# Performance work log

Hardware: AMD Instinct MI355X
Metric: run time of the kernel (lower is better)

The kernel has to match this reference:

```python
import jax, jax.numpy as jnp
import numpy as np
import math

B, C, H, W = 16, 128, 64, 64

def _conv3(x, w, b):
    # 3x3 conv, padding=1 (SAME), NCHW / OIHW
    y = jax.lax.conv_general_dilated(x, w, window_strides=(1, 1), padding='SAME',
                                     dimension_numbers=('NCHW', 'OIHW', 'NCHW'))
    return y + b[None, :, None, None]

def setup_inputs() -> dict:
    key = jax.random.key(0)
    ks = jax.random.split(key, 12)
    s = 0.02
    inp = {
        'F_in': jax.random.normal(ks[0], (B, C, H, W), dtype=jnp.float32),
        'Pspe': jax.random.normal(ks[1], (B, C, C), dtype=jnp.float32),
        'q_w': jax.random.normal(ks[2], (C, C, 3, 3), dtype=jnp.float32) * s,
        'q_b': jnp.zeros((C,), dtype=jnp.float32),
        'k_w': jax.random.normal(ks[3], (C, C, 3, 3), dtype=jnp.float32) * s,
        'k_b': jnp.zeros((C,), dtype=jnp.float32),
        'v_w': jax.random.normal(ks[4], (C, C, 3, 3), dtype=jnp.float32) * s,
        'v_b': jnp.zeros((C,), dtype=jnp.float32),
        'f1_w': jax.random.normal(ks[5], (C, C, 3, 3), dtype=jnp.float32) * s,
        'f1_b': jnp.zeros((C,), dtype=jnp.float32),
        'f2_w': jax.random.normal(ks[6], (C, C, 3, 3), dtype=jnp.float32) * s,
        'f2_b': jnp.zeros((C,), dtype=jnp.float32),
    }
    return inp

def reference(F_in, Pspe, q_w, q_b, k_w, k_b, v_w, v_b, f1_w, f1_b, f2_w, f2_b):
    b, c, h, w = F_in.shape
    hw = h * w
    Qm = _conv3(F_in, q_w, q_b)
    Km = _conv3(F_in, k_w, k_b)
    Vm = _conv3(F_in, v_w, v_b)
    # (B,C,H,W) -> (B,HW,C)
    Q = jnp.transpose(Qm, (0, 2, 3, 1)).reshape(b, hw, c)
    K = jnp.transpose(Km, (0, 2, 3, 1)).reshape(b, hw, c)
    V = jnp.transpose(Vm, (0, 2, 3, 1)).reshape(b, hw, c)
    # channel-wise attention: (B,C,C) = K^T Q, contracting over HW
    attn_logits = jnp.einsum('bnc,bnd->bcd', K, Q) / math.sqrt(hw)
    A = jax.nn.softmax(attn_logits, axis=-1)
    M = jnp.einsum('bce,bed->bcd', Pspe, A)         # prompt fusion
    F3 = jnp.einsum('bnc,bcd->bnd', V, M)           # (B,HW,C)
    F3_map = jnp.transpose(F3.reshape(b, h, w, c), (0, 3, 1, 2))
    # MScanBlock is not defined in the provided source -> identity
    F_ssm = F3_map
    ffn = _conv3(jax.nn.gelu(_conv3(F_ssm, f1_w, f1_b), approximate=False), f2_w, f2_b)
    return F_ssm + ffn
```

## Files before the change

### kernel.cpp

```cpp
#include <hip/hip_runtime.h>
#include <cmath>

typedef unsigned short u16;
typedef __bf16 bf16x8 __attribute__((ext_vector_type(8)));
typedef float f32x4 __attribute__((ext_vector_type(4)));

__device__ __forceinline__ u16 f2bf(float f) {
  unsigned u = __float_as_uint(f);
  u += 0x7fffu + ((u >> 16) & 1u);
  return (u16)(u >> 16);
}
__device__ __forceinline__ float bf2f(u16 h) {
  return __uint_as_float(((unsigned)h) << 16);
}
__device__ __forceinline__ f32x4 mfma_bf16(bf16x8 a, bf16x8 b, f32x4 c) {
  return __builtin_amdgcn_mfma_f32_16x16x32_bf16(a, b, c, 0, 0, 0);
}
__device__ __forceinline__ float gelu_exact(float x) {
  return 0.5f * x * (1.0f + erff(x * 0.70710678118654752440f));
}

#define VMCNT2() asm volatile("s_waitcnt vmcnt(2)" ::: "memory")
#define VMCNT0() asm volatile("s_waitcnt vmcnt(0)" ::: "memory")
#define BARR()                                  \
  do {                                          \
    asm volatile("" ::: "memory");              \
    __builtin_amdgcn_s_barrier();               \
    asm volatile("" ::: "memory");              \
  } while (0)

__device__ __forceinline__ void gload16(const void* g, void* l) {
  __builtin_amdgcn_global_load_lds(
      (const __attribute__((address_space(1))) unsigned*)g,
      (__attribute__((address_space(3))) unsigned*)l, 16, 0, 0);
}

__device__ __forceinline__ size_t pidx(int b, int y, int x) {
  return ((size_t)(b * 66 + y) * 66 + x) * 128;
}

__device__ __forceinline__ void border_yx(int k, int& y, int& x) {
  if (k < 66) { y = 0; x = k; }
  else if (k < 132) { y = 65; x = k - 66; }
  else if (k < 196) { y = k - 131; x = 0; }
  else { y = k - 195; x = 65; }
}

__global__ __launch_bounds__(256) void pack_xw(
    const float* __restrict__ Fin, u16* __restrict__ Xp,
    const float* __restrict__ w0, const float* __restrict__ w1,
    const float* __restrict__ w2, const float* __restrict__ w3,
    const float* __restrict__ w4, u16* __restrict__ Wpk) {
  const int tid = threadIdx.x;
  const int bid = blockIdx.x;
  if (bid < 1024) {
    __shared__ float T[64 * 129];
    const int b = bid >> 6, y = bid & 63;
#pragma unroll
    for (int i = 0; i < 32; ++i) {
      int idx = tid + i * 256;
      int c = idx >> 6, x = idx & 63;
      T[x * 129 + c] = Fin[(size_t)(b * 128 + c) * 4096 + y * 64 + x];
    }
    __syncthreads();
#pragma unroll
    for (int i = 0; i < 4; ++i) {
      int chunk = tid + i * 256;
      int x = chunk >> 4;
      int c0 = (chunk & 15) * 8;
      u16 tmp[8];
#pragma unroll
      for (int e = 0; e < 8; ++e) tmp[e] = f2bf(T[x * 129 + c0 + e]);
      *reinterpret_cast<uint4*>(Xp + pidx(b, y + 1, x + 1) + c0) =
          *reinterpret_cast<const uint4*>(tmp);
    }
  } else if (bid < 1384) {
    int gid = (bid - 1024) * 256 + tid;
    int lane = gid & 63;
    int nblk = (gid >> 6) & 7;
    int step = (gid >> 9) % 36;
    int conv = gid / (512 * 36);
    if (conv >= 5) return;
    const float* w = conv == 0 ? w0 : conv == 1 ? w1 : conv == 2 ? w2 : conv == 3 ? w3 : w4;
    int tap = step >> 2, cc = step & 3;
    int dy = tap / 3, dx = tap % 3;
    int co = nblk * 16 + (lane & 15);
    int ci0 = cc * 32 + (lane >> 4) * 8;
    u16 tmp[8];
#pragma unroll
    for (int e = 0; e < 8; ++e)
      tmp[e] = f2bf(w[((size_t)(co * 128 + ci0 + e) * 3 + dy) * 3 + dx]);
    size_t off = ((size_t)conv * 36 * 8 * 64 + (size_t)((step * 8 + nblk) * 64 + lane)) * 8;
    *reinterpret_cast<uint4*>(Wpk + off) = *reinterpret_cast<const uint4*>(tmp);
  } else {
    int p = (bid - 1384) * 16 + (tid >> 4);
    int b = p / 260, k = p % 260;
    int y, x;
    border_yx(k, y, x);
    *reinterpret_cast<uint4*>(Xp + pidx(b, y, x) + (tid & 15) * 8) =
        make_uint4(0u, 0u, 0u, 0u);
  }
}

template <int MODE>
__global__ __launch_bounds__(256, 2) void conv5(
    const u16* __restrict__ Xin, const u16* __restrict__ Wp0,
    const float* __restrict__ bq, const float* __restrict__ bk,
    const float* __restrict__ bv,
    u16* __restrict__ O0, u16* __restrict__ O1, u16* __restrict__ O2,
    float* __restrict__ OutF, const u16* __restrict__ Resid) {
  __shared__ alignas(16) char smem[58368];
  char* Abuf = smem;
  char* Bring = smem + 33792;
  const int tid = threadIdx.x;
  const int lane = tid & 63, wv = tid >> 6;
  const int wm = wv >> 1, wn = wv & 1;
  const int lm = lane & 15, lq = lane >> 4;
  const int bid = blockIdx.x;
  const int cv = (MODE == 0) ? (bid >> 9) : 0;
  const int mtr = bid & 511;
  const int mt = (mtr & 7) * 64 + (mtr >> 3);
  const int b = mt >> 5, yp = mt & 31;
  const u16* WpC = Wp0 + (size_t)cv * 147456;

  f32x4 acc[4][4];
#pragma unroll
  for (int i = 0; i < 4; ++i)
#pragma unroll
    for (int j = 0; j < 4; ++j) acc[i][j] = f32x4{0.f, 0.f, 0.f, 0.f};

  auto stageA = [&](int h) {
#pragma unroll
    for (int r = 0; r < 9; ++r) {
      int c = wv * 528 + r * 64 + lane;
      int row = c >> 3, c16 = c & 7;
      int ys = row / 66, xs = row - ys * 66;
      const u16* src =
          Xin + pidx(b, yp * 2 + ys, xs) + h * 64 + ((c16 ^ (xs & 7)) << 3);
      char* dst = Abuf + (wv * 528 + r * 64) * 16;
      if (r < 8)
        gload16(src, dst);
      else if (lane < 16)
        gload16(src, dst);
    }
  };
  auto stageB = [&](int t, int h) {
    int ws = (t >> 1) * 4 + h * 2 + (t & 1);
    const u16* s0 = WpC + (size_t)ws * 4096 + (size_t)(wv * 128 + lane) * 8;
    char* d0 = Bring + (t % 3) * 8192 + wv * 2048;
    gload16(s0, d0);
    gload16(s0 + 512, d0 + 1024);
  };

#pragma unroll 1
  for (int h = 0; h < 2; ++h) {
    BARR();
    stageA(h);
    stageB(0, h);
    stageB(1, h);
    VMCNT2();
    BARR();
#pragma unroll
    for (int t = 0; t < 18; ++t) {
      if (t > 0) {
        if (t < 17) VMCNT2(); else VMCNT0();
        BARR();
      }
      if (t + 2 < 18) stageB(t + 2, h);
      const int tap = t >> 1, ccL = t & 1;
      const int dy = tap / 3, dx = tap % 3;
      bf16x8 af[4], bfr[4];
#pragma unroll
      for (int i = 0; i < 4; ++i) {
        int p = wm * 64 + i * 16 + lm;
        int xs = (p & 63) + dx, ys = (p >> 6) + dy;
        unsigned off = (unsigned)(((ys * 66 + xs) * 64 + ccL * 32 + lq * 8) * 2) ^
                       (unsigned)((xs & 7) << 4);
        af[i] = *reinterpret_cast<const bf16x8*>(Abuf + off);
      }
      const char* bb = Bring + (t % 3) * 8192;
#pragma unroll
      for (int j = 0; j < 4; ++j)
        bfr[j] = *reinterpret_cast<const bf16x8*>(
            bb + ((wn * 4 + j) * 64 + lane) * 16);
#pragma unroll
      for (int i = 0; i < 4; ++i)
#pragma unroll
        for (int j = 0; j < 4; ++j) acc[i][j] = mfma_bf16(af[i], bfr[j], acc[i][j]);
    }
  }

  __syncthreads();

  if (MODE == 0 && cv < 2) {
    const float* bias = cv == 0 ? bq : bk;
    u16* OutB = cv == 0 ? O0 : O1;
    u16* T = (u16*)smem;
#pragma unroll
    for (int i = 0; i < 4; ++i)
#pragma unroll
      for (int j = 0; j < 4; ++j) {
        int n = wn * 64 + j * 16 + lm;
        float bs = bias[n];
#pragma unroll
        for (int r = 0; r < 4; ++r) {
          int m = wm * 64 + i * 16 + lq * 4 + r;
          T[n * 136 + m] = f2bf(acc[i][j][r] + bs);
        }
      }
    __syncthreads();
#pragma unroll
    for (int it = 0; it < 8; ++it) {
      int item = tid + it * 256;
      int l = item & 63, cb = (item >> 6) & 7, ksl = item >> 9;
      int c = cb * 16 + (l & 15);
      int mloc = ksl * 32 + (l >> 4) * 8;
      int ks = yp * 4 + ksl;
      *reinterpret_cast<uint4*>(
          OutB + (size_t)(((b * 128 + ks) * 8 + cb) * 64 + l) * 8) =
          *reinterpret_cast<const uint4*>(T + c * 136 + mloc);
    }
  } else if (MODE == 0) {
    u16* T = (u16*)smem;
#pragma unroll
    for (int i = 0; i < 4; ++i)
#pragma unroll
      for (int j = 0; j < 4; ++j) {
        int n = wn * 64 + j * 16 + lm;
        float bs = bv[n];
#pragma unroll
        for (int r = 0; r < 4; ++r) {
          int m = wm * 64 + i * 16 + lq * 4 + r;
          T[m * 136 + n] = f2bf(acc[i][j][r] + bs);
        }
      }
    __syncthreads();
    int rr = tid >> 1, hf = tid & 1;
    const uint4* src = reinterpret_cast<const uint4*>(T + rr * 136 + hf * 64);
    uint4* dst = reinterpret_cast<uint4*>(O2 + ((size_t)(mt * 128 + rr) * 128 + hf * 64));
#pragma unroll
    for (int k = 0; k < 8; ++k) dst[k] = src[k];
  } else if (MODE == 1) {
    u16* T = (u16*)smem;
#pragma unroll
    for (int i = 0; i < 4; ++i)
#pragma unroll
      for (int j = 0; j < 4; ++j) {
        int n = wn * 64 + j * 16 + lm;
        float bs = bq[n];
#pragma unroll
        for (int r = 0; r < 4; ++r) {
          int m = wm * 64 + i * 16 + lq * 4 + r;
          T[m * 136 + n] = f2bf(gelu_exact(acc[i][j][r] + bs));
        }
      }
    __syncthreads();
    int rr = tid >> 1, hf = tid & 1;
    int y = yp * 2 + (rr >> 6), x = rr & 63;
    const uint4* src = reinterpret_cast<const uint4*>(T + rr * 136 + hf * 64);
    uint4* dst = reinterpret_cast<uint4*>(O0 + pidx(b, y + 1, x + 1) + hf * 64);
#pragma unroll
    for (int k = 0; k < 8; ++k) dst[k] = src[k];
  } else {
    float* Tf = (float*)smem;
#pragma unroll
    for (int jh = 0; jh < 2; ++jh) {
      if (jh) __syncthreads();
#pragma unroll
      for (int i = 0; i < 4; ++i)
#pragma unroll
        for (int j2 = 0; j2 < 2; ++j2) {
          int j = jh * 2 + j2;
          int n = wn * 64 + j * 16 + lm;
          int nl = wn * 32 + j2 * 16 + lm;
          float bs = bq[n];
          int m0 = wm * 64 + i * 16 + lq * 4;
          int y = yp * 2 + (m0 >> 6), x = m0 & 63;
          const u16* rp = Resid + pidx(b, y + 1, x + 1) + n;
#pragma unroll
          for (int r = 0; r < 4; ++r)
            Tf[nl * 132 + m0 + r] = acc[i][j][r] + bs + bf2f(rp[r * 128]);
        }
      __syncthreads();
      int nl = tid >> 2, seg = tid & 3;
      int gn = (nl >> 5) * 64 + jh * 32 + (nl & 31);
      float* dst = OutF + ((size_t)(b * 128 + gn) * 4096 + yp * 128 + seg * 32);
      const float* src = Tf + nl * 132 + seg * 32;
#pragma unroll
      for (int k = 0; k < 8; ++k)
        reinterpret_cast<float4*>(dst)[k] = reinterpret_cast<const float4*>(src)[k];
    }
  }
}

__global__ __launch_bounds__(256, 2) void attn_s(const u16* __restrict__ QP,
                                                 const u16* __restrict__ KP,
                                                 float* __restrict__ SP) {
  const int tid = threadIdx.x;
  const int lane = tid & 63;
  const int wv = tid >> 6, wm = wv >> 1, wn = wv & 1;
  const int lm = lane & 15, lq = lane >> 4;
  int mt = blockIdx.x;
  mt = (mt & 7) * 16 + (mt >> 3);
  const int b = mt >> 3, sp = mt & 7;

  f32x4 acc[4][4];
#pragma unroll
  for (int i = 0; i < 4; ++i)
#pragma unroll
    for (int j = 0; j < 4; ++j) acc[i][j] = f32x4{0.f, 0.f, 0.f, 0.f};

#pragma unroll
  for (int ksl = 0; ksl < 16; ++ksl) {
    const int ks = sp * 16 + ksl;
    bf16x8 af[4], bfr[4];
#pragma unroll
    for (int i = 0; i < 4; ++i)
      af[i] = *reinterpret_cast<const bf16x8*>(
          KP + (size_t)(((b * 128 + ks) * 8 + wm * 4 + i) * 64 + lane) * 8);
#pragma unroll
    for (int j = 0; j < 4; ++j)
      bfr[j] = *reinterpret_cast<const bf16x8*>(
          QP + (size_t)(((b * 128 + ks) * 8 + wn * 4 + j) * 64 + lane) * 8);
#pragma unroll
    for (int i = 0; i < 4; ++i)
#pragma unroll
      for (int j = 0; j < 4; ++j) acc[i][j] = mfma_bf16(af[i], bfr[j], acc[i][j]);
  }

  float* out = SP + (size_t)(b * 8 + sp) * 16384;
#pragma unroll
  for (int i = 0; i < 4; ++i)
#pragma unroll
    for (int j = 0; j < 4; ++j)
#pragma unroll
      for (int r = 0; r < 4; ++r)
        out[(wm * 64 + i * 16 + lq * 4 + r) * 128 + wn * 64 + j * 16 + lm] =
            acc[i][j][r];
}

__global__ __launch_bounds__(256) void attn_r(const float* __restrict__ SP,
                                              u16* __restrict__ ABP) {
  __shared__ float Sf[32][129];
  __shared__ float Inv[32];
  const int tid = threadIdx.x;
  const int b = blockIdx.x >> 2, eb = blockIdx.x & 3;

#pragma unroll
  for (int it = 0; it < 16; ++it) {
    int id = it * 256 + tid;
    int rl = id >> 7, d = id & 127;
    const float* p = SP + (size_t)b * 8 * 16384 + (size_t)(eb * 32 + rl) * 128 + d;
    float s = 0.f;
#pragma unroll
    for (int sp = 0; sp < 8; ++sp) s += p[(size_t)sp * 16384];
    Sf[rl][d] = s * 0.015625f;
  }
  __syncthreads();

  {
    int rl = tid >> 3, sub = tid & 7;
    float mx = -3.4e38f;
#pragma unroll
    for (int k = 0; k < 16; ++k) mx = fmaxf(mx, Sf[rl][sub + 8 * k]);
    mx = fmaxf(mx, __shfl_xor(mx, 1));
    mx = fmaxf(mx, __shfl_xor(mx, 2));
    mx = fmaxf(mx, __shfl_xor(mx, 4));
    float s = 0.f;
#pragma unroll
    for (int k = 0; k < 16; ++k) {
      float e = __expf(Sf[rl][sub + 8 * k] - mx);
      Sf[rl][sub + 8 * k] = e;
      s += e;
    }
    s += __shfl_xor(s, 1);
    s += __shfl_xor(s, 2);
    s += __shfl_xor(s, 4);
    if (sub == 0) Inv[rl] = 1.0f / s;
  }
  __syncthreads();

#pragma unroll
  for (int it = 0; it < 2; ++it) {
    int item = tid + it * 256;
    int l = item & 63, nb = item >> 6;
    int d = nb * 16 + (l & 15);
    u16 tmp[8];
#pragma unroll
    for (int e = 0; e < 8; ++e) {
      int rloc = (l >> 4) * 8 + e;
      tmp[e] = f2bf(Sf[rloc][d] * Inv[rloc]);
    }
    *reinterpret_cast<uint4*>(ABP + (size_t)(((b * 4 + eb) * 8 + nb) * 64 + l) * 8) =
        *reinterpret_cast<const uint4*>(tmp);
  }
}

__global__ __launch_bounds__(256, 1) void attn_m(const float* __restrict__ Pspe,
                                                 const u16* __restrict__ ABP,
                                                 u16* __restrict__ Mpack) {
  __shared__ u16 Ml[128 * 136];
  const int b = blockIdx.x;
  const int tid = threadIdx.x;
  const int lane = tid & 63;
  const int wv = tid >> 6, wm = wv >> 1, wn = wv & 1;
  const int lm = lane & 15, lq = lane >> 4;

  f32x4 acc[4][4];
#pragma unroll
  for (int i = 0; i < 4; ++i)
#pragma unroll
    for (int j = 0; j < 4; ++j) acc[i][j] = f32x4{0.f, 0.f, 0.f, 0.f};

  const float* P = Pspe + (size_t)b * 128 * 128;
#pragma unroll
  for (int cc = 0; cc < 4; ++cc) {
    int e0 = cc * 32 + lq * 8;
    bf16x8 af[4], bfr[4];
#pragma unroll
    for (int i = 0; i < 4; ++i) {
      const float* p = P + (size_t)(wm * 64 + i * 16 + lm) * 128 + e0;
      union { u16 u[8]; bf16x8 v; } cvu;
#pragma unroll
      for (int e = 0; e < 8; ++e) cvu.u[e] = f2bf(p[e]);
      af[i] = cvu.v;
    }
#pragma unroll
    for (int j = 0; j < 4; ++j)
      bfr[j] = *reinterpret_cast<const bf16x8*>(
          ABP + (size_t)(((b * 4 + cc) * 8 + wn * 4 + j) * 64 + lane) * 8);
#pragma unroll
    for (int i = 0; i < 4; ++i)
#pragma unroll
      for (int j = 0; j < 4; ++j) acc[i][j] = mfma_bf16(af[i], bfr[j], acc[i][j]);
  }

#pragma unroll
  for (int i = 0; i < 4; ++i)
#pragma unroll
    for (int j = 0; j < 4; ++j)
#pragma unroll
      for (int r = 0; r < 4; ++r)
        Ml[(wn * 64 + j * 16 + lm) * 136 + (wm * 64 + i * 16 + lq * 4 + r)] =
            f2bf(acc[i][j][r]);
  __syncthreads();

#pragma unroll
  for (int it = 0; it < 8; ++it) {
    int item = tid + it * 256;
    int l2 = item & 63, nb = (item >> 6) & 7, cc2 = item >> 9;
    int d = nb * 16 + (l2 & 15), c0 = cc2 * 32 + (l2 >> 4) * 8;
    *reinterpret_cast<uint4*>(Mpack + (size_t)b * 16384 + (size_t)item * 8) =
        *reinterpret_cast<const uint4*>(Ml + d * 136 + c0);
  }
}

__global__ __launch_bounds__(256) void f3_gemm(const u16* __restrict__ V,
                                               const u16* __restrict__ Mpack,
                                               u16* __restrict__ Fp,
                                               u16* __restrict__ Hp) {
  const int tid = threadIdx.x;
  const int lane = tid & 63;
  const int wv = tid >> 6, wm = wv >> 1, wn = wv & 1;
  const int lm = lane & 15, lq = lane >> 4;
  const int bid = blockIdx.x;
  int mt = bid;
  mt = (mt & 7) * 64 + (mt >> 3);
  const int b = mt >> 5;
  const int yp = mt & 31;

  f32x4 acc[4][4];
#pragma unroll
  for (int i = 0; i < 4; ++i)
#pragma unroll
    for (int j = 0; j < 4; ++j) acc[i][j] = f32x4{0.f, 0.f, 0.f, 0.f};

#pragma unroll
  for (int cc = 0; cc < 4; ++cc) {
    int k0 = cc * 32 + lq * 8;
    bf16x8 af[4], bfr[4];
#pragma unroll
    for (int i = 0; i < 4; ++i)
      af[i] = *reinterpret_cast<const bf16x8*>(
          V + (size_t)(mt * 128 + wm * 64 + i * 16 + lm) * 128 + k0);
#pragma unroll
    for (int j = 0; j < 4; ++j)
      bfr[j] = *reinterpret_cast<const bf16x8*>(
          Mpack + (size_t)b * 16384 + (size_t)((cc * 8 + wn * 4 + j) * 64 + lane) * 8);
#pragma unroll
    for (int i = 0; i < 4; ++i)
#pragma unroll
      for (int j = 0; j < 4; ++j) acc[i][j] = mfma_bf16(af[i], bfr[j], acc[i][j]);
  }

#pragma unroll
  for (int rep = 0; rep < 2; ++rep) {
    int p = bid * 32 + rep * 16 + (tid >> 4);
    if (p < 8320) {
      u16* buf = p < 4160 ? Fp : Hp;
      int q = p < 4160 ? p : p - 4160;
      int bb = q / 260, k = q % 260;
      int y, x;
      border_yx(k, y, x);
      *reinterpret_cast<uint4*>(buf + pidx(bb, y, x) + (tid & 15) * 8) =
          make_uint4(0u, 0u, 0u, 0u);
    }
  }

  __shared__ u16 T[128 * 136];
#pragma unroll
  for (int i = 0; i < 4; ++i)
#pragma unroll
    for (int j = 0; j < 4; ++j)
#pragma unroll
      for (int r = 0; r < 4; ++r)
        T[(wm * 64 + i * 16 + lq * 4 + r) * 136 + wn * 64 + j * 16 + lm] =
            f2bf(acc[i][j][r]);
  __syncthreads();
  int rr = tid >> 1, hf = tid & 1;
  int y = yp * 2 + (rr >> 6), x = rr & 63;
  const uint4* src = reinterpret_cast<const uint4*>(T + rr * 136 + hf * 64);
  uint4* dst = reinterpret_cast<uint4*>(Fp + pidx(b, y + 1, x + 1) + hf * 64);
#pragma unroll
  for (int k = 0; k < 8; ++k) dst[k] = src[k];
}

extern "C" void kernel_launch(void* const* d_in, const int* in_sizes, int n_in,
                              void* d_out, int out_size, void* d_ws, size_t ws_size,
                              hipStream_t stream) {
  const float* F_in = (const float*)d_in[0];
  const float* Pspe = (const float*)d_in[1];
  const float* q_w = (const float*)d_in[2];
  const float* q_b = (const float*)d_in[3];
  const float* k_w = (const float*)d_in[4];
  const float* k_b = (const float*)d_in[5];
  const float* v_w = (const float*)d_in[6];
  const float* v_b = (const float*)d_in[7];
  const float* f1_w = (const float*)d_in[8];
  const float* f1_b = (const float*)d_in[9];
  const float* f2_w = (const float*)d_in[10];
  const float* f2_b = (const float*)d_in[11];
  float* out = (float*)d_out;

  char* ws = (char*)d_ws;
  const size_t XPO = 0;
  const size_t QPO = 17842176;
  const size_t KPO = QPO + 16777216;
  const size_t VO  = KPO + 16777216;
  const size_t WPO = VO + 16777216;

  u16* Xp = (u16*)(ws + XPO);
  u16* QP = (u16*)(ws + QPO);
  u16* KP = (u16*)(ws + KPO);
  u16* V = (u16*)(ws + VO);
  u16* Wpk = (u16*)(ws + WPO);
  float* SP = (float*)(ws + XPO);
  u16* ABP = KP;
  u16* Mpk = (u16*)(ws + KPO + 1179648);
  u16* Fp = Xp;
  u16* Hp = QP;

  pack_xw<<<1644, 256, 0, stream>>>(F_in, Xp, q_w, k_w, v_w, f1_w, f2_w, Wpk);
  conv5<0><<<1536, 256, 0, stream>>>(Xp, Wpk, q_b, k_b, v_b, QP, KP, V, nullptr, nullptr);
  attn_s<<<128, 256, 0, stream>>>(QP, KP, SP);
  attn_r<<<64, 256, 0, stream>>>(SP, ABP);
  attn_m<<<16, 256, 0, stream>>>(Pspe, ABP, Mpk);
  f3_gemm<<<512, 256, 0, stream>>>(V, Mpk, Fp, Hp);
  conv5<1><<<512, 256, 0, stream>>>(Fp, Wpk + 3 * 147456, f1_b, nullptr, nullptr,
                                    Hp, nullptr, nullptr, nullptr, nullptr);
  conv5<2><<<512, 256, 0, stream>>>(Hp, Wpk + 4 * 147456, f2_b, nullptr, nullptr,
                                    nullptr, nullptr, nullptr, out, Fp);
}
```

Measured before the change: 171.6 us.

## Load conv weight fragments straight from global and split FFN convs across N

Drops the triple-buffered LDS ring for conv weight tiles and its explicit vmcnt/barrier pipeline. Each wave now reads its pre-packed bf16 weight fragments directly from global memory (L2) into registers. This shrinks LDS so launch bounds can rise to 4 blocks per CU. The f1/f2 FFN convs are also split into two 64-channel output halves, doubling their grid and halving per-block accumulators, which trades repeated activation staging for more parallelism. The risk is that global weight-load latency is no longer hidden by the LDS prefetch ring.

```diff
diff --git a/kernel.cpp b/kernel.cpp
--- a/kernel.cpp
+++ b/kernel.cpp
@@ -19,15 +19,6 @@
 __device__ __forceinline__ float gelu_exact(float x) {
   return 0.5f * x * (1.0f + erff(x * 0.70710678118654752440f));
 }
-
-#define VMCNT2() asm volatile("s_waitcnt vmcnt(2)" ::: "memory")
-#define VMCNT0() asm volatile("s_waitcnt vmcnt(0)" ::: "memory")
-#define BARR()                                  \
-  do {                                          \
-    asm volatile("" ::: "memory");              \
-    __builtin_amdgcn_s_barrier();               \
-    asm volatile("" ::: "memory");              \
-  } while (0)
 
 __device__ __forceinline__ void gload16(const void* g, void* l) {
   __builtin_amdgcn_global_load_lds(
@@ -102,32 +93,35 @@
   }
 }
 
-template <int MODE>
-__global__ __launch_bounds__(256, 2) void conv5(
+template <int MODE, int NS>
+__global__ __launch_bounds__(256, 4) void conv5(
     const u16* __restrict__ Xin, const u16* __restrict__ Wp0,
     const float* __restrict__ bq, const float* __restrict__ bk,
     const float* __restrict__ bv,
     u16* __restrict__ O0, u16* __restrict__ O1, u16* __restrict__ O2,
     float* __restrict__ OutF, const u16* __restrict__ Resid) {
-  __shared__ alignas(16) char smem[58368];
+  constexpr int NBJ = 4 / NS;
+  __shared__ alignas(16) char smem[MODE == 0 ? 34816 : 33792];
   char* Abuf = smem;
-  char* Bring = smem + 33792;
   const int tid = threadIdx.x;
   const int lane = tid & 63, wv = tid >> 6;
   const int wm = wv >> 1, wn = wv & 1;
   const int lm = lane & 15, lq = lane >> 4;
   const int bid = blockIdx.x;
   const int cv = (MODE == 0) ? (bid >> 9) : 0;
-  const int mtr = bid & 511;
+  const int nh = (NS == 2) ? (bid & 1) : 0;
+  const int mtr = (MODE == 0) ? (bid & 511) : (bid >> 1);
   const int mt = (mtr & 7) * 64 + (mtr >> 3);
   const int b = mt >> 5, yp = mt & 31;
   const u16* WpC = Wp0 + (size_t)cv * 147456;
-
-  f32x4 acc[4][4];
-#pragma unroll
-  for (int i = 0; i < 4; ++i)
-#pragma unroll
-    for (int j = 0; j < 4; ++j) acc[i][j] = f32x4{0.f, 0.f, 0.f, 0.f};
+  const int cb0 = nh * 4 + wn * NBJ;
+  const u16* wlane = WpC + (size_t)cb0 * 512 + (size_t)lane * 8;
+
+  f32x4 acc[4][NBJ];
+#pragma unroll
+  for (int i = 0; i < 4; ++i)
+#pragma unroll
+    for (int j = 0; j < NBJ; ++j) acc[i][j] = f32x4{0.f, 0.f, 0.f, 0.f};
 
   auto stageA = [&](int h) {
 #pragma unroll
@@ -144,49 +138,34 @@
         gload16(src, dst);
     }
   };
-  auto stageB = [&](int t, int h) {
-    int ws = (t >> 1) * 4 + h * 2 + (t & 1);
-    const u16* s0 = WpC + (size_t)ws * 4096 + (size_t)(wv * 128 + lane) * 8;
-    char* d0 = Bring + (t % 3) * 8192 + wv * 2048;
-    gload16(s0, d0);
-    gload16(s0 + 512, d0 + 1024);
-  };
 
 #pragma unroll 1
   for (int h = 0; h < 2; ++h) {
-    BARR();
+    __syncthreads();
     stageA(h);
-    stageB(0, h);
-    stageB(1, h);
-    VMCNT2();
-    BARR();
+    __syncthreads();
 #pragma unroll
     for (int t = 0; t < 18; ++t) {
-      if (t > 0) {
-        if (t < 17) VMCNT2(); else VMCNT0();
-        BARR();
-      }
-      if (t + 2 < 18) stageB(t + 2, h);
       const int tap = t >> 1, ccL = t & 1;
-      const int dy = tap / 3, dx = tap % 3;
-      bf16x8 af[4], bfr[4];
+      const int dy = tap / 3, dx = tap - dy * 3;
+      const int ws = tap * 4 + h * 2 + ccL;
+      const int ysrow = (wm + dy) * 8448;
+      const int q0 = ccL * 4 + lq;
+      bf16x8 af[4], bfr[NBJ];
 #pragma unroll
       for (int i = 0; i < 4; ++i) {
-        int p = wm * 64 + i * 16 + lm;
-        int xs = (p & 63) + dx, ys = (p >> 6) + dy;
-        unsigned off = (unsigned)(((ys * 66 + xs) * 64 + ccL * 32 + lq * 8) * 2) ^
-                       (unsigned)((xs & 7) << 4);
+        int xs = i * 16 + lm + dx;
+        int off = ysrow + xs * 128 + ((q0 ^ (xs & 7)) << 4);
         af[i] = *reinterpret_cast<const bf16x8*>(Abuf + off);
       }
-      const char* bb = Bring + (t % 3) * 8192;
-#pragma unroll
-      for (int j = 0; j < 4; ++j)
-        bfr[j] = *reinterpret_cast<const bf16x8*>(
-            bb + ((wn * 4 + j) * 64 + lane) * 16);
+#pragma unroll
+      for (int j = 0; j < NBJ; ++j)
+        bfr[j] = *reinterpret_cast<const bf16x8*>(wlane + ws * 4096 + j * 512);
 #pragma unroll
       for (int i = 0; i < 4; ++i)
 #pragma unroll
-        for (int j = 0; j < 4; ++j) acc[i][j] = mfma_bf16(af[i], bfr[j], acc[i][j]);
+        for (int j = 0; j < NBJ; ++j)
+          acc[i][j] = mfma_bf16(af[i], bfr[j], acc[i][j]);
     }
   }
 
@@ -199,7 +178,7 @@
 #pragma unroll
     for (int i = 0; i < 4; ++i)
 #pragma unroll
-      for (int j = 0; j < 4; ++j) {
+      for (int j = 0; j < NBJ; ++j) {
         int n = wn * 64 + j * 16 + lm;
         float bs = bias[n];
 #pragma unroll
@@ -225,7 +204,7 @@
 #pragma unroll
     for (int i = 0; i < 4; ++i)
 #pragma unroll
-      for (int j = 0; j < 4; ++j) {
+      for (int j = 0; j < NBJ; ++j) {
         int n = wn * 64 + j * 16 + lm;
         float bs = bv[n];
 #pragma unroll
@@ -245,51 +224,46 @@
 #pragma unroll
     for (int i = 0; i < 4; ++i)
 #pragma unroll
-      for (int j = 0; j < 4; ++j) {
-        int n = wn * 64 + j * 16 + lm;
-        float bs = bq[n];
+      for (int j = 0; j < NBJ; ++j) {
+        int nloc = wn * 32 + j * 16 + lm;
+        float bs = bq[nh * 64 + nloc];
 #pragma unroll
         for (int r = 0; r < 4; ++r) {
           int m = wm * 64 + i * 16 + lq * 4 + r;
-          T[m * 136 + n] = f2bf(gelu_exact(acc[i][j][r] + bs));
+          T[m * 72 + nloc] = f2bf(gelu_exact(acc[i][j][r] + bs));
         }
       }
     __syncthreads();
-    int rr = tid >> 1, hf = tid & 1;
+    int rr = tid >> 1, q = tid & 1;
     int y = yp * 2 + (rr >> 6), x = rr & 63;
-    const uint4* src = reinterpret_cast<const uint4*>(T + rr * 136 + hf * 64);
-    uint4* dst = reinterpret_cast<uint4*>(O0 + pidx(b, y + 1, x + 1) + hf * 64);
-#pragma unroll
-    for (int k = 0; k < 8; ++k) dst[k] = src[k];
+    const uint4* src = reinterpret_cast<const uint4*>(T + rr * 72 + q * 32);
+    uint4* dst =
+        reinterpret_cast<uint4*>(O0 + pidx(b, y + 1, x + 1) + nh * 64 + q * 32);
+#pragma unroll
+    for (int k = 0; k < 4; ++k) dst[k] = src[k];
   } else {
     float* Tf = (float*)smem;
 #pragma unroll
-    for (int jh = 0; jh < 2; ++jh) {
-      if (jh) __syncthreads();
-#pragma unroll
-      for (int i = 0; i < 4; ++i)
-#pragma unroll
-        for (int j2 = 0; j2 < 2; ++j2) {
-          int j = jh * 2 + j2;
-          int n = wn * 64 + j * 16 + lm;
-          int nl = wn * 32 + j2 * 16 + lm;
-          float bs = bq[n];
-          int m0 = wm * 64 + i * 16 + lq * 4;
-          int y = yp * 2 + (m0 >> 6), x = m0 & 63;
-          const u16* rp = Resid + pidx(b, y + 1, x + 1) + n;
-#pragma unroll
-          for (int r = 0; r < 4; ++r)
-            Tf[nl * 132 + m0 + r] = acc[i][j][r] + bs + bf2f(rp[r * 128]);
-        }
-      __syncthreads();
-      int nl = tid >> 2, seg = tid & 3;
-      int gn = (nl >> 5) * 64 + jh * 32 + (nl & 31);
-      float* dst = OutF + ((size_t)(b * 128 + gn) * 4096 + yp * 128 + seg * 32);
-      const float* src = Tf + nl * 132 + seg * 32;
-#pragma unroll
-      for (int k = 0; k < 8; ++k)
-        reinterpret_cast<float4*>(dst)[k] = reinterpret_cast<const float4*>(src)[k];
-    }
+    for (int i = 0; i < 4; ++i)
+#pragma unroll
+      for (int j = 0; j < NBJ; ++j) {
+        int nl = wn * 32 + j * 16 + lm;
+        int n = nh * 64 + nl;
+        float bs = bq[n];
+        int m0 = wm * 64 + i * 16 + lq * 4;
+        int y = yp * 2 + (m0 >> 6), x = m0 & 63;
+        const u16* rp = Resid + pidx(b, y + 1, x + 1) + n;
+#pragma unroll
+        for (int r = 0; r < 4; ++r)
+          Tf[nl * 132 + m0 + r] = acc[i][j][r] + bs + bf2f(rp[r * 128]);
+      }
+    __syncthreads();
+    int nl = tid >> 2, seg = tid & 3;
+    float* dst = OutF + ((size_t)(b * 128 + nh * 64 + nl) * 4096 + yp * 128 + seg * 32);
+    const float* src = Tf + nl * 132 + seg * 32;
+#pragma unroll
+    for (int k = 0; k < 8; ++k)
+      reinterpret_cast<float4*>(dst)[k] = reinterpret_cast<const float4*>(src)[k];
   }
 }
 
@@ -561,13 +535,16 @@
   u16* Hp = QP;
 
   pack_xw<<<1644, 256, 0, stream>>>(F_in, Xp, q_w, k_w, v_w, f1_w, f2_w, Wpk);
-  conv5<0><<<1536, 256, 0, stream>>>(Xp, Wpk, q_b, k_b, v_b, QP, KP, V, nullptr, nullptr);
+  conv5<0, 1><<<1536, 256, 0, stream>>>(Xp, Wpk, q_b, k_b, v_b, QP, KP, V,
+                                        nullptr, nullptr);
   attn_s<<<128, 256, 0, stream>>>(QP, KP, SP);
   attn_r<<<64, 256, 0, stream>>>(SP, ABP);
   attn_m<<<16, 256, 0, stream>>>(Pspe, ABP, Mpk);
   f3_gemm<<<512, 256, 0, stream>>>(V, Mpk, Fp, Hp);
-  conv5<1><<<512, 256, 0, stream>>>(Fp, Wpk + 3 * 147456, f1_b, nullptr, nullptr,
-                                    Hp, nullptr, nullptr, nullptr, nullptr);
-  conv5<2><<<512, 256, 0, stream>>>(Hp, Wpk + 4 * 147456, f2_b, nullptr, nullptr,
-                                    nullptr, nullptr, nullptr, out, Fp);
-}
+  conv5<1, 2><<<1024, 256, 0, stream>>>(Fp, Wpk + 3 * 147456, f1_b, nullptr,
+                                        nullptr, Hp, nullptr, nullptr, nullptr,
+                                        nullptr);
+  conv5<2, 2><<<1024, 256, 0, stream>>>(Hp, Wpk + 4 * 147456, f2_b, nullptr,
+                                        nullptr, nullptr, nullptr, nullptr, out,
+                                        Fp);
+}
```

Result: slower. 196.6 us (+14.5%).
